# Performance work log

Hardware: AMD Instinct MI355X
Metric: run time of the kernel (lower is better)

The kernel has to match this reference:

```python
import jax, jax.numpy as jnp
import numpy as np

B, T, F = 128, 64, 2048
N, H, C = 1024, 1024, 22  # neurons, hidden_size, num_classes


def setup_inputs() -> dict:
    key = jax.random.key(0)
    ks = jax.random.split(key, 9)
    def w(k, shape, fan_in):
        return jax.random.normal(k, shape, dtype=jnp.float32) / np.sqrt(fan_in)
    return {
        "x": jax.random.normal(ks[0], (B, T, F), dtype=jnp.float32),
        "W1": w(ks[1], (N, F), F),
        "b1": jnp.zeros((N,), jnp.float32),
        "W_ih": w(ks[2], (4 * H, N), N),
        "b_ih": jnp.zeros((4 * H,), jnp.float32),
        "W_hh": w(ks[3], (4 * H, H), H),
        "b_hh": jnp.zeros((4 * H,), jnp.float32),
        "Wc": w(ks[4], (C, H), H),
        "bc": jnp.zeros((C,), jnp.float32),
    }


def reference(x, W1, b1, W_ih, b_ih, W_hh, b_hh, Wc, bc):
    b, t, _ = x.shape
    h0 = jnp.zeros((b, H), x.dtype)
    c0 = jnp.zeros((b, H), x.dtype)
    # Precompute the input-side projections for every step (batched GEMMs):
    z = jax.nn.relu(jnp.einsum("btf,nf->btn", x, W1) + b1)        # [B,T,N]
    xg = jnp.einsum("btn,gn->btg", z, W_ih) + b_ih                 # [B,T,4H]

    def step(carry, xg_t):
        h, c = carry
        gates = xg_t + h @ W_hh.T + b_hh                           # [B,4H]
        i, f, g, o = jnp.split(gates, 4, axis=-1)                  # torch LSTMCell gate order
        c = jax.nn.sigmoid(f) * c + jax.nn.sigmoid(i) * jnp.tanh(g)
        h = jax.nn.sigmoid(o) * jnp.tanh(c)
        return (h, c), h

    _, hs = jax.lax.scan(step, (h0, c0), jnp.swapaxes(xg, 0, 1))    # hs: [T,B,H]
    scores = jnp.einsum("tbh,ch->tbc", hs, Wc) + bc                # [T,B,C]
    scores = jnp.swapaxes(scores, 0, 1).reshape(-1, Wc.shape[0])    # [B*T, C]
    return scores
```

## Files before the change

### kernel.cpp

```cpp
#include <hip/hip_runtime.h>
#include <hip/hip_bf16.h>

typedef short bf16x8 __attribute__((ext_vector_type(8)));
typedef float f32x4 __attribute__((ext_vector_type(4)));

#define B_ 128
#define T_ 64
#define F_ 2048
#define N_ 1024
#define H_ 1024
#define C_ 22

__device__ __forceinline__ ushort f2bf(float f) {
    union { float f; unsigned u; } v; v.f = f;
    unsigned u = v.u;
    unsigned r = (u + 0x7FFFu + ((u >> 16) & 1u)) >> 16;
    return (ushort)r;
}
__device__ __forceinline__ float bf2f(ushort h) {
    union { unsigned u; float f; } v; v.u = ((unsigned)h) << 16;
    return v.f;
}

__global__ __launch_bounds__(256) void cvt_f32_bf16(const float* __restrict__ in,
                                                    ushort* __restrict__ out, int n4) {
    int i = blockIdx.x * blockDim.x + threadIdx.x;
    if (i < n4) {
        float4 v = ((const float4*)in)[i];
        ushort4 o;
        o.x = f2bf(v.x); o.y = f2bf(v.y); o.z = f2bf(v.z); o.w = f2bf(v.w);
        ((ushort4*)out)[i] = o;
    }
}

__global__ __launch_bounds__(256) void cvt_wc(const float* __restrict__ Wc,
                                              ushort* __restrict__ Wcb) {
    int i = blockIdx.x * 256 + threadIdx.x;
    int row = i >> 10;
    Wcb[i] = (row < C_) ? f2bf(Wc[i]) : (ushort)0;
}

__device__ __forceinline__ void gload16(const void* g, void* l) {
    __builtin_amdgcn_global_load_lds(
        (const __attribute__((address_space(1))) unsigned int*)g,
        (__attribute__((address_space(3))) unsigned int*)l, 16, 0, 0);
}

template<int K, bool RELU>
__global__ __launch_bounds__(256) void gemm_bt(const ushort* __restrict__ A,
                                               const ushort* __restrict__ Bm,
                                               const float* __restrict__ bias1,
                                               const float* __restrict__ bias2,
                                               ushort* __restrict__ C,
                                               int Nt, int Nn) {
    __shared__ ushort sA[128 * 32];
    __shared__ ushort sB[128 * 32];
    const int tid = threadIdx.x;
    const int lane = tid & 63, wv = tid >> 6;
    const int tm = blockIdx.x / Nt, tn = blockIdx.x % Nt;
    const int wm = wv >> 1, wn = wv & 1;

    const ushort* gA = A + (size_t)(tm * 128 + (tid >> 2)) * K + (tid & 3) * 8;
    const ushort* gB = Bm + (size_t)(tn * 128 + (tid >> 2)) * K + (tid & 3) * 8;
    char* lAb = (char*)sA + wv * 1024;
    char* lBb = (char*)sB + wv * 1024;

    f32x4 acc[4][4] = {};

    for (int kt = 0; kt < K / 32; kt++) {
        const ushort* a0 = gA + kt * 32;
        const ushort* b0 = gB + kt * 32;
        gload16(a0, lAb);
        gload16(a0 + 64 * K, lAb + 4096);
        gload16(b0, lBb);
        gload16(b0 + 64 * K, lBb + 4096);
        __syncthreads();

        bf16x8 af[4], bfv[4];
#pragma unroll
        for (int i = 0; i < 4; i++)
            af[i] = *(const bf16x8*)&sA[(wm * 64 + i * 16 + (lane & 15)) * 32 + (lane >> 4) * 8];
#pragma unroll
        for (int j = 0; j < 4; j++)
            bfv[j] = *(const bf16x8*)&sB[(wn * 64 + j * 16 + (lane & 15)) * 32 + (lane >> 4) * 8];
#pragma unroll
        for (int i = 0; i < 4; i++)
#pragma unroll
            for (int j = 0; j < 4; j++)
                acc[i][j] = __builtin_amdgcn_mfma_f32_16x16x32_bf16(af[i], bfv[j], acc[i][j], 0, 0, 0);
        __syncthreads();
    }

#pragma unroll
    for (int j = 0; j < 4; j++) {
        int n = tn * 128 + wn * 64 + j * 16 + (lane & 15);
        float bias = bias1[n] + (bias2 ? bias2[n] : 0.f);
#pragma unroll
        for (int i = 0; i < 4; i++) {
            int mbase = tm * 128 + wm * 64 + i * 16 + (lane >> 4) * 4;
#pragma unroll
            for (int r = 0; r < 4; r++) {
                float v = acc[i][j][r] + bias;
                if (RELU) v = v > 0.f ? v : 0.f;
                C[(size_t)(mbase + r) * Nn + n] = f2bf(v);
            }
        }
    }
}

__global__ __launch_bounds__(512, 2) void lstm_persist(ushort* __restrict__ hs,
                                                       const ushort* __restrict__ xg,
                                                       const ushort* __restrict__ Whh,
                                                       unsigned* __restrict__ flags) {
    const int tid = threadIdx.x;
    const int lane = tid & 63;
    const int wv = tid >> 6;
    const int g = wv >> 1;
    const int ch = wv & 1;
    const int blk = (int)blockIdx.x;
    const int bt = blk & 7;
    const int hb = blk >> 3;
    const int batch0 = bt * 16;
    const int hid0 = hb * 32;

    bf16x8 breg[32];
    {
        const ushort* br = Whh + (size_t)(g * H_ + hid0 + ch * 16 + (lane & 15)) * H_
                         + ((lane >> 4) * 8);
#pragma unroll
        for (int ks = 0; ks < 32; ks++) breg[ks] = *(const bf16x8*)(br + ks * 32);
#pragma unroll
        for (int ks = 0; ks < 32; ks++) asm volatile("" : "+v"(breg[ks]));
    }

    __shared__ float lg[4][16][32];

    const int grow = tid >> 5;
    const int gcol = tid & 31;
    const int b = batch0 + grow;
    const int jj = hid0 + gcol;
    const ushort* xrow = xg + ((size_t)(b * T_) << 12) + jj;
    float c0 = 0.f;

    for (int t = 0; t < T_; t++) {
        const ushort* xr = xrow + ((size_t)t << 12);
        ushort xi = xr[0], xf = xr[1024], xgv = xr[2048], xo = xr[3072];

        const ushort* ar = hs + (size_t)t * (B_ * H_)
                         + (size_t)(batch0 + (lane & 15)) * H_ + ((lane >> 4) * 8);
        f32x4 acc = {};
#pragma unroll
        for (int ks = 0; ks < 32; ks++) {
            bf16x8 a0 = *(const bf16x8*)(ar + ks * 32);
            acc = __builtin_amdgcn_mfma_f32_16x16x32_bf16(a0, breg[ks], acc, 0, 0, 0);
        }
#pragma unroll
        for (int r = 0; r < 4; r++)
            lg[g][(lane >> 4) * 4 + r][ch * 16 + (lane & 15)] = acc[r];
        __syncthreads();

        {
            float pi = bf2f(xi)  + lg[0][grow][gcol];
            float pf = bf2f(xf)  + lg[1][grow][gcol];
            float pg = bf2f(xgv) + lg[2][grow][gcol];
            float po = bf2f(xo)  + lg[3][grow][gcol];
            float si = 1.f / (1.f + expf(-pi));
            float sf = 1.f / (1.f + expf(-pf));
            float tg = tanhf(pg);
            float so = 1.f / (1.f + expf(-po));
            c0 = sf * c0 + si * tg;
            ushort hbf = f2bf(so * tanhf(c0));
            uint other = __shfl_xor((uint)hbf, 1);
            if ((lane & 1) == 0) {
                uint hp = (uint)hbf | (other << 16);
                unsigned* hp32 = (unsigned*)(hs + (size_t)(t + 1) * (B_ * H_)
                                             + (size_t)b * H_ + jj);
                __hip_atomic_store(hp32, hp, __ATOMIC_RELAXED, __HIP_MEMORY_SCOPE_AGENT);
            }
        }
        __syncthreads();

        if (t < T_ - 1) {
            if (tid == 0)
                __hip_atomic_store(&flags[blk * 16], (unsigned)(t + 1),
                                   __ATOMIC_RELAXED, __HIP_MEMORY_SCOPE_AGENT);
            if (wv == 0) {
                asm volatile("s_waitcnt vmcnt(0)" ::: "memory");
                for (;;) {
                    unsigned f = __hip_atomic_load(&flags[((lane & 31) * 8 + bt) * 16],
                                                   __ATOMIC_RELAXED, __HIP_MEMORY_SCOPE_AGENT);
                    if (__ballot(f < (unsigned)(t + 1)) == 0ull) break;
                    __builtin_amdgcn_s_sleep(1);
                }
            }
            __syncthreads();
        }
    }
}

__global__ __launch_bounds__(256) void scores_mfma(const ushort* __restrict__ hs,
                                                   const ushort* __restrict__ Wcb,
                                                   const float* __restrict__ bc,
                                                   float* __restrict__ out) {
    const int tid = threadIdx.x, lane = tid & 63, w = tid >> 6;
    const int r0 = blockIdx.x * 64 + w * 16;
    const int rr = r0 + (lane & 15);
    const int b = rr >> 6, t = rr & 63;
    const ushort* arow = hs + (size_t)(t + 1) * (B_ * H_) + (size_t)b * H_ + ((lane >> 4) * 8);
    const ushort* brow0 = Wcb + (size_t)(lane & 15) * H_ + ((lane >> 4) * 8);
    const ushort* brow1 = brow0 + 16 * H_;

    f32x4 acc0 = {}, acc1 = {};
#pragma unroll
    for (int ks = 0; ks < 32; ks++) {
        bf16x8 a  = *(const bf16x8*)(arow + ks * 32);
        bf16x8 p0 = *(const bf16x8*)(brow0 + ks * 32);
        bf16x8 p1 = *(const bf16x8*)(brow1 + ks * 32);
        acc0 = __builtin_amdgcn_mfma_f32_16x16x32_bf16(a, p0, acc0, 0, 0, 0);
        acc1 = __builtin_amdgcn_mfma_f32_16x16x32_bf16(a, p1, acc1, 0, 0, 0);
    }
#pragma unroll
    for (int nf = 0; nf < 2; nf++) {
        int c = nf * 16 + (lane & 15);
        if (c < C_) {
            float bias = bc[c];
            f32x4 acc = nf ? acc1 : acc0;
#pragma unroll
            for (int r = 0; r < 4; r++) {
                int row = r0 + (lane >> 4) * 4 + r;
                out[(size_t)row * C_ + c] = acc[r] + bias;
            }
        }
    }
}

extern "C" void kernel_launch(void* const* d_in, const int* in_sizes, int n_in,
                              void* d_out, int out_size, void* d_ws, size_t ws_size,
                              hipStream_t stream) {
    const float* x = (const float*)d_in[0];
    const float* W1 = (const float*)d_in[1];
    const float* b1 = (const float*)d_in[2];
    const float* W_ih = (const float*)d_in[3];
    const float* b_ih = (const float*)d_in[4];
    const float* W_hh = (const float*)d_in[5];
    const float* b_hh = (const float*)d_in[6];
    const float* Wc = (const float*)d_in[7];
    const float* bc = (const float*)d_in[8];
    float* out = (float*)d_out;

    char* ws = (char*)d_ws;
    ushort* Xb   = (ushort*)(ws);
    ushort* W1b  = (ushort*)(ws + 33554432);
    ushort* Wihb = (ushort*)(ws + 37748736);
    ushort* Whhb = (ushort*)(ws + 46137344);
    ushort* z    = (ushort*)(ws + 54525952);
    ushort* xg   = (ushort*)(ws + 71303168);
    ushort* hs   = (ushort*)(ws + 138412032);
    ushort* Wcb  = (ushort*)(ws + 155451392);
    unsigned* flags = (unsigned*)(ws + 155516928);

    hipMemsetAsync(hs, 0, (size_t)B_ * H_ * sizeof(ushort), stream);
    hipMemsetAsync(flags, 0, 16384, stream);

    cvt_f32_bf16<<<16384, 256, 0, stream>>>(x, Xb, 4194304);
    cvt_f32_bf16<<<2048, 256, 0, stream>>>(W1, W1b, 524288);
    cvt_f32_bf16<<<4096, 256, 0, stream>>>(W_ih, Wihb, 1048576);
    cvt_f32_bf16<<<4096, 256, 0, stream>>>(W_hh, Whhb, 1048576);
    cvt_wc<<<128, 256, 0, stream>>>(Wc, Wcb);

    gemm_bt<2048, true><<<512, 256, 0, stream>>>(Xb, W1b, b1, nullptr, z, 8, 1024);
    gemm_bt<1024, false><<<2048, 256, 0, stream>>>(z, Wihb, b_ih, b_hh, xg, 32, 4096);

    lstm_persist<<<256, 512, 0, stream>>>(hs, xg, Whhb, flags);

    scores_mfma<<<128, 256, 0, stream>>>(hs, Wcb, bc, out);
}
```

Baseline: 820.6 us.

## Repartition persistent LSTM to 64 blocks covering 64 batch rows each

The persistent LSTM kernel moves from 256 blocks (16 batch rows by 32 hidden units each) to 64 blocks (64 batch rows by 32 hidden units). Each wave now runs four interleaved MFMA accumulation chains per step, and each thread handles a 2x2 tile with vectorized xg loads. Gate activations switch to __expf-based sigmoid and tanh, and the vmcnt wait moves before the block barrier so all waves' h stores drain before the flag is raised. The aim is to cut redundant hs reads and activation cost, at the price of more serial MFMA work per block on fewer CUs.

```diff
diff --git a/kernel.cpp b/kernel.cpp
--- a/kernel.cpp
+++ b/kernel.cpp
@@ -21,6 +21,8 @@
     union { unsigned u; float f; } v; v.u = ((unsigned)h) << 16;
     return v.f;
 }
+__device__ __forceinline__ float sigm_f(float x) { return 1.f / (1.f + __expf(-x)); }
+__device__ __forceinline__ float tanh_f(float x) { return 1.f - 2.f / (1.f + __expf(2.f * x)); }
 
 __global__ __launch_bounds__(256) void cvt_f32_bf16(const float* __restrict__ in,
                                                     ushort* __restrict__ out, int n4) {
@@ -118,10 +120,10 @@
     const int g = wv >> 1;
     const int ch = wv & 1;
     const int blk = (int)blockIdx.x;
-    const int bt = blk & 7;
-    const int hb = blk >> 3;
-    const int batch0 = bt * 16;
-    const int hid0 = hb * 32;
+    const int bh = blk & 1;
+    const int cb = blk >> 1;
+    const int batch0 = bh * 64;
+    const int hid0 = cb * 32;
 
     bf16x8 breg[32];
     {
@@ -133,51 +135,63 @@
         for (int ks = 0; ks < 32; ks++) asm volatile("" : "+v"(breg[ks]));
     }
 
-    __shared__ float lg[4][16][32];
-
-    const int grow = tid >> 5;
-    const int gcol = tid & 31;
-    const int b = batch0 + grow;
-    const int jj = hid0 + gcol;
-    const ushort* xrow = xg + ((size_t)(b * T_) << 12) + jj;
-    float c0 = 0.f;
+    __shared__ float lg[4][64][33];
+
+    const int cp = tid & 15;
+    const int rg = tid >> 4;
+    const int row0 = rg * 2;
+    const int b0g = batch0 + row0;
+    const int jj = hid0 + cp * 2;
+    float c_[4] = {0.f, 0.f, 0.f, 0.f};
 
     for (int t = 0; t < T_; t++) {
-        const ushort* xr = xrow + ((size_t)t << 12);
-        ushort xi = xr[0], xf = xr[1024], xgv = xr[2048], xo = xr[3072];
-
-        const ushort* ar = hs + (size_t)t * (B_ * H_)
-                         + (size_t)(batch0 + (lane & 15)) * H_ + ((lane >> 4) * 8);
-        f32x4 acc = {};
-#pragma unroll
-        for (int ks = 0; ks < 32; ks++) {
-            bf16x8 a0 = *(const bf16x8*)(ar + ks * 32);
-            acc = __builtin_amdgcn_mfma_f32_16x16x32_bf16(a0, breg[ks], acc, 0, 0, 0);
-        }
-#pragma unroll
-        for (int r = 0; r < 4; r++)
-            lg[g][(lane >> 4) * 4 + r][ch * 16 + (lane & 15)] = acc[r];
-        __syncthreads();
-
-        {
-            float pi = bf2f(xi)  + lg[0][grow][gcol];
-            float pf = bf2f(xf)  + lg[1][grow][gcol];
-            float pg = bf2f(xgv) + lg[2][grow][gcol];
-            float po = bf2f(xo)  + lg[3][grow][gcol];
-            float si = 1.f / (1.f + expf(-pi));
-            float sf = 1.f / (1.f + expf(-pf));
-            float tg = tanhf(pg);
-            float so = 1.f / (1.f + expf(-po));
-            c0 = sf * c0 + si * tg;
-            ushort hbf = f2bf(so * tanhf(c0));
-            uint other = __shfl_xor((uint)hbf, 1);
-            if ((lane & 1) == 0) {
-                uint hp = (uint)hbf | (other << 16);
-                unsigned* hp32 = (unsigned*)(hs + (size_t)(t + 1) * (B_ * H_)
-                                             + (size_t)b * H_ + jj);
-                __hip_atomic_store(hp32, hp, __ATOMIC_RELAXED, __HIP_MEMORY_SCOPE_AGENT);
-            }
-        }
+        uint xv[4][2];
+#pragma unroll
+        for (int g2 = 0; g2 < 4; g2++)
+#pragma unroll
+            for (int i = 0; i < 2; i++)
+                xv[g2][i] = *(const uint*)(xg + (((size_t)(b0g + i) * T_ + t) << 12)
+                                           + g2 * H_ + jj);
+
+#pragma unroll
+        for (int sp = 0; sp < 2; sp++) {
+            const ushort* ar = hs + (size_t)t * (B_ * H_)
+                             + (size_t)(batch0 + sp * 32 + (lane & 15)) * H_ + ((lane >> 4) * 8);
+            f32x4 acc0 = {}, acc1 = {};
+#pragma unroll
+            for (int ks = 0; ks < 32; ks++) {
+                bf16x8 a0 = *(const bf16x8*)(ar + ks * 32);
+                bf16x8 a1 = *(const bf16x8*)(ar + 16 * H_ + ks * 32);
+                acc0 = __builtin_amdgcn_mfma_f32_16x16x32_bf16(a0, breg[ks], acc0, 0, 0, 0);
+                acc1 = __builtin_amdgcn_mfma_f32_16x16x32_bf16(a1, breg[ks], acc1, 0, 0, 0);
+            }
+#pragma unroll
+            for (int r = 0; r < 4; r++) {
+                lg[g][sp * 32 + (lane >> 4) * 4 + r][ch * 16 + (lane & 15)] = acc0[r];
+                lg[g][sp * 32 + 16 + (lane >> 4) * 4 + r][ch * 16 + (lane & 15)] = acc1[r];
+            }
+        }
+        __syncthreads();
+
+#pragma unroll
+        for (int i = 0; i < 2; i++) {
+            float h2[2];
+#pragma unroll
+            for (int j = 0; j < 2; j++) {
+                float pi = bf2f((ushort)(xv[0][i] >> (16 * j))) + lg[0][row0 + i][cp * 2 + j];
+                float pf = bf2f((ushort)(xv[1][i] >> (16 * j))) + lg[1][row0 + i][cp * 2 + j];
+                float pg = bf2f((ushort)(xv[2][i] >> (16 * j))) + lg[2][row0 + i][cp * 2 + j];
+                float po = bf2f((ushort)(xv[3][i] >> (16 * j))) + lg[3][row0 + i][cp * 2 + j];
+                float& cc = c_[i * 2 + j];
+                cc = sigm_f(pf) * cc + sigm_f(pi) * tanh_f(pg);
+                h2[j] = sigm_f(po) * tanh_f(cc);
+            }
+            uint hp = (uint)f2bf(h2[0]) | ((uint)f2bf(h2[1]) << 16);
+            unsigned* hp32 = (unsigned*)(hs + (size_t)(t + 1) * (B_ * H_)
+                                         + (size_t)(b0g + i) * H_ + jj);
+            __hip_atomic_store(hp32, hp, __ATOMIC_RELAXED, __HIP_MEMORY_SCOPE_AGENT);
+        }
+        asm volatile("s_waitcnt vmcnt(0)" ::: "memory");
         __syncthreads();
 
         if (t < T_ - 1) {
@@ -185,9 +199,8 @@
                 __hip_atomic_store(&flags[blk * 16], (unsigned)(t + 1),
                                    __ATOMIC_RELAXED, __HIP_MEMORY_SCOPE_AGENT);
             if (wv == 0) {
-                asm volatile("s_waitcnt vmcnt(0)" ::: "memory");
                 for (;;) {
-                    unsigned f = __hip_atomic_load(&flags[((lane & 31) * 8 + bt) * 16],
+                    unsigned f = __hip_atomic_load(&flags[(((lane & 31) * 2) + bh) * 16],
                                                    __ATOMIC_RELAXED, __HIP_MEMORY_SCOPE_AGENT);
                     if (__ballot(f < (unsigned)(t + 1)) == 0ull) break;
                     __builtin_amdgcn_s_sleep(1);
@@ -271,7 +284,7 @@
     gemm_bt<2048, true><<<512, 256, 0, stream>>>(Xb, W1b, b1, nullptr, z, 8, 1024);
     gemm_bt<1024, false><<<2048, 256, 0, stream>>>(z, Wihb, b_ih, b_hh, xg, 32, 4096);
 
-    lstm_persist<<<256, 512, 0, stream>>>(hs, xg, Whhb, flags);
+    lstm_persist<<<64, 512, 0, stream>>>(hs, xg, Whhb, flags);
 
     scores_mfma<<<128, 256, 0, stream>>>(hs, Wcb, bc, out);
 }
```

Measured after the change: 2.151 ms. 2.62x slower.

## Use XCC-local workgroup-scope flags for LSTM step barrier when group shares die

Applied to the files above, without the earlier changes.

At kernel start, each block records its XCC id. The lead block of each batch group checks whether all 32 blocks in that group sit on the same XCC and publishes the decision. If they do, hidden-state stores and step flags use workgroup-scope atomics, and polling uses fetch_add, to avoid agent-scope (cross-die) coherence traffic. It falls back to agent-scope flags on a timeout. This adds a startup handshake and relies on memory-scope behaviour across CUs within one XCC, which is a correctness risk.

```diff
diff --git a/kernel.cpp b/kernel.cpp
--- a/kernel.cpp
+++ b/kernel.cpp
@@ -111,7 +111,10 @@
 __global__ __launch_bounds__(512, 2) void lstm_persist(ushort* __restrict__ hs,
                                                        const ushort* __restrict__ xg,
                                                        const ushort* __restrict__ Whh,
-                                                       unsigned* __restrict__ flags) {
+                                                       unsigned* __restrict__ flagL,
+                                                       unsigned* __restrict__ flagA,
+                                                       unsigned* __restrict__ xcctab,
+                                                       unsigned* __restrict__ decis) {
     const int tid = threadIdx.x;
     const int lane = tid & 63;
     const int wv = tid >> 6;
@@ -123,6 +126,38 @@
     const int batch0 = bt * 16;
     const int hid0 = hb * 32;
 
+    __shared__ int s_local;
+
+    unsigned myxcc;
+    asm volatile("s_getreg_b32 %0, hwreg(HW_REG_XCC_ID)" : "=s"(myxcc));
+    if (tid == 0)
+        __hip_atomic_store(&xcctab[blk], myxcc + 1, __ATOMIC_RELAXED, __HIP_MEMORY_SCOPE_AGENT);
+    if (blk == bt && wv == 0) {
+        unsigned ok = 2u;
+        for (int it = 0; it < 100000; ++it) {
+            unsigned e = __hip_atomic_load(&xcctab[(lane & 31) * 8 + bt],
+                                           __ATOMIC_RELAXED, __HIP_MEMORY_SCOPE_AGENT);
+            if (__ballot(e == 0u) == 0ull) {
+                ok = (__ballot(e != myxcc + 1) == 0ull) ? 1u : 2u;
+                break;
+            }
+            __builtin_amdgcn_s_sleep(2);
+        }
+        if (lane == 0)
+            __hip_atomic_store(&decis[bt], ok, __ATOMIC_RELAXED, __HIP_MEMORY_SCOPE_AGENT);
+    }
+    if (wv == 0) {
+        unsigned dec;
+        for (;;) {
+            dec = __hip_atomic_load(&decis[bt], __ATOMIC_RELAXED, __HIP_MEMORY_SCOPE_AGENT);
+            if (__ballot(dec == 0u) == 0ull) break;
+            __builtin_amdgcn_s_sleep(2);
+        }
+        if (lane == 0) s_local = (dec == 1u);
+    }
+    __syncthreads();
+    const bool local = (s_local != 0);
+
     bf16x8 breg[32];
     {
         const ushort* br = Whh + (size_t)(g * H_ + hid0 + ch * 16 + (lane & 15)) * H_
@@ -141,6 +176,10 @@
     const int jj = hid0 + gcol;
     const ushort* xrow = xg + ((size_t)(b * T_) << 12) + jj;
     float c0 = 0.f;
+
+    unsigned* fLp = &flagL[(((lane & 31) * 8) + bt) * 16];
+    unsigned* fAp = &flagA[(((lane & 31) * 8) + bt) * 16];
+    bool useA = !local;
 
     for (int t = 0; t < T_; t++) {
         const ushort* xr = xrow + ((size_t)t << 12);
@@ -175,22 +214,41 @@
                 uint hp = (uint)hbf | (other << 16);
                 unsigned* hp32 = (unsigned*)(hs + (size_t)(t + 1) * (B_ * H_)
                                              + (size_t)b * H_ + jj);
-                __hip_atomic_store(hp32, hp, __ATOMIC_RELAXED, __HIP_MEMORY_SCOPE_AGENT);
-            }
-        }
+                if (local)
+                    __hip_atomic_store(hp32, hp, __ATOMIC_RELAXED, __HIP_MEMORY_SCOPE_WORKGROUP);
+                else
+                    __hip_atomic_store(hp32, hp, __ATOMIC_RELAXED, __HIP_MEMORY_SCOPE_AGENT);
+            }
+        }
+        asm volatile("s_waitcnt vmcnt(0)" ::: "memory");
         __syncthreads();
 
         if (t < T_ - 1) {
-            if (tid == 0)
-                __hip_atomic_store(&flags[blk * 16], (unsigned)(t + 1),
+            if (tid == 0) {
+                if (local)
+                    __hip_atomic_store(&flagL[blk * 16], (unsigned)(t + 1),
+                                       __ATOMIC_RELAXED, __HIP_MEMORY_SCOPE_WORKGROUP);
+                __hip_atomic_store(&flagA[blk * 16], (unsigned)(t + 1),
                                    __ATOMIC_RELAXED, __HIP_MEMORY_SCOPE_AGENT);
+            }
             if (wv == 0) {
-                asm volatile("s_waitcnt vmcnt(0)" ::: "memory");
-                for (;;) {
-                    unsigned f = __hip_atomic_load(&flags[((lane & 31) * 8 + bt) * 16],
-                                                   __ATOMIC_RELAXED, __HIP_MEMORY_SCOPE_AGENT);
-                    if (__ballot(f < (unsigned)(t + 1)) == 0ull) break;
-                    __builtin_amdgcn_s_sleep(1);
+                if (!useA) {
+                    int sweeps = 0;
+                    for (;;) {
+                        unsigned f = __hip_atomic_fetch_add(fLp, 0u,
+                                         __ATOMIC_RELAXED, __HIP_MEMORY_SCOPE_WORKGROUP);
+                        if (__ballot(f < (unsigned)(t + 1)) == 0ull) break;
+                        if (++sweeps > 20000) { useA = true; break; }
+                        __builtin_amdgcn_s_sleep(1);
+                    }
+                }
+                if (useA) {
+                    for (;;) {
+                        unsigned f = __hip_atomic_load(fAp,
+                                         __ATOMIC_RELAXED, __HIP_MEMORY_SCOPE_AGENT);
+                        if (__ballot(f < (unsigned)(t + 1)) == 0ull) break;
+                        __builtin_amdgcn_s_sleep(1);
+                    }
                 }
             }
             __syncthreads();
@@ -257,10 +315,16 @@
     ushort* xg   = (ushort*)(ws + 71303168);
     ushort* hs   = (ushort*)(ws + 138412032);
     ushort* Wcb  = (ushort*)(ws + 155451392);
-    unsigned* flags = (unsigned*)(ws + 155516928);
+    unsigned* flagL  = (unsigned*)(ws + 155516928);
+    unsigned* flagA  = (unsigned*)(ws + 155533312);
+    unsigned* xcctab = (unsigned*)(ws + 155549696);
+    unsigned* decis  = (unsigned*)(ws + 155550720);
 
     hipMemsetAsync(hs, 0, (size_t)B_ * H_ * sizeof(ushort), stream);
-    hipMemsetAsync(flags, 0, 16384, stream);
+    hipMemsetAsync(flagL, 0, 16384, stream);
+    hipMemsetAsync(flagA, 0, 16384, stream);
+    hipMemsetAsync(xcctab, 0, 1024, stream);
+    hipMemsetAsync(decis, 0, 1024, stream);
 
     cvt_f32_bf16<<<16384, 256, 0, stream>>>(x, Xb, 4194304);
     cvt_f32_bf16<<<2048, 256, 0, stream>>>(W1, W1b, 524288);
@@ -271,7 +335,7 @@
     gemm_bt<2048, true><<<512, 256, 0, stream>>>(Xb, W1b, b1, nullptr, z, 8, 1024);
     gemm_bt<1024, false><<<2048, 256, 0, stream>>>(z, Wihb, b_ih, b_hh, xg, 32, 4096);
 
-    lstm_persist<<<256, 512, 0, stream>>>(hs, xg, Whhb, flags);
+    lstm_persist<<<256, 512, 0, stream>>>(hs, xg, Whhb, flagL, flagA, xcctab, decis);
 
     scores_mfma<<<128, 256, 0, stream>>>(hs, Wcb, bc, out);
 }
```

After: 2.995 ms. 265% more time.
